# Optimization experiments

Hardware: AMD Instinct MI355X
Metric: run time of the kernel (lower is better)

The kernel has to match this reference:

```python
import jax, jax.numpy as jnp
import numpy as np

B, S, H = 32, 2048, 1024

def setup_inputs() -> dict:
    key = jax.random.key(0)
    k1, k2, k3, k4 = jax.random.split(key, 4)
    scale_w = 1.0 / np.sqrt(3 * H)
    scale_v = 1.0 / np.sqrt(H)
    return {
        "enc_output": jax.random.normal(k1, (B, S, 2 * H), dtype=jnp.float32),
        "enc_mask": jnp.ones((B, S, 1), dtype=jnp.float32),
        "dec_hidden": jax.random.normal(k2, (1, B, H), dtype=jnp.float32),
        "W_w": jax.random.normal(k3, (H, 3 * H), dtype=jnp.float32) * scale_w,
        "W_b": jnp.zeros((H,), dtype=jnp.float32),
        "V_w": jax.random.normal(k4, (1, H), dtype=jnp.float32) * scale_v,
        "V_b": jnp.zeros((1,), dtype=jnp.float32),
    }


def reference(enc_output, enc_mask, dec_hidden, W_w, W_b, V_w, V_b):
    # enc_output: (B, S, 2H); enc_mask: (B, S, 1); dec_hidden: (1, B, H)
    b, s, _ = enc_output.shape
    h = dec_hidden.shape[-1]
    dec = jnp.broadcast_to(jnp.transpose(dec_hidden, (1, 0, 2)), (b, s, h))  # (B,S,H)
    x = jnp.concatenate([enc_output, dec], axis=-1)                          # (B,S,3H)
    energy = jnp.tanh(jnp.einsum('bsk,hk->bsh', x, W_w) + W_b)               # (B,S,H)
    scores = jnp.einsum('bsh,oh->bso', energy, V_w)[..., 0] + V_b[0]         # (B,S)
    keep = enc_mask[..., 0] > 0  # original masks where (1 - mask) is True
    scores = jnp.where(keep, scores, -jnp.inf)
    attn = jax.nn.softmax(scores, axis=-1)                                   # (B,S)
    context = jnp.einsum('bs,bsd->bd', attn, enc_output)                     # (B,2H)
    return context
```

## Files before the change

### kernel.cpp

```cpp
#include <hip/hip_runtime.h>
#include <hip/hip_bf16.h>
#include <math.h>

#define B_   32
#define S_   2048
#define H_   1024
#define K2H  2048
#define M_TOT (B_*S_)

typedef __attribute__((ext_vector_type(8))) short bf16x8;
typedef __attribute__((ext_vector_type(4))) float f32x4;

__device__ __forceinline__ short f2bf(float f) {
    union { float f; unsigned u; } c; c.f = f;
    unsigned u = c.u;
    unsigned r = u + 0x7FFFu + ((u >> 16) & 1u);
    return (short)(r >> 16);
}

__global__ void convert_enc(const float* __restrict__ enc, short* __restrict__ encb) {
    size_t e = ((size_t)blockIdx.x * blockDim.x + threadIdx.x) * 8;
    float4 v0 = *reinterpret_cast<const float4*>(enc + e);
    float4 v1 = *reinterpret_cast<const float4*>(enc + e + 4);
    short s[8];
    s[0]=f2bf(v0.x); s[1]=f2bf(v0.y); s[2]=f2bf(v0.z); s[3]=f2bf(v0.w);
    s[4]=f2bf(v1.x); s[5]=f2bf(v1.y); s[6]=f2bf(v1.z); s[7]=f2bf(v1.w);
    *reinterpret_cast<int4*>(encb + e) = *reinterpret_cast<const int4*>(s);
}

__global__ void convert_w1(const float* __restrict__ W, short* __restrict__ w1) {
    int idx = blockIdx.x * blockDim.x + threadIdx.x;
    int e = idx * 4;
    int h = e >> 11;
    int k = e & 2047;
    float4 v = *reinterpret_cast<const float4*>(W + (size_t)h * 3072 + k);
    short4 o;
    o.x = f2bf(v.x); o.y = f2bf(v.y); o.z = f2bf(v.z); o.w = f2bf(v.w);
    *reinterpret_cast<short4*>(w1 + (size_t)h * 2048 + k) = o;
}

__global__ void dproj_kernel(const float* __restrict__ dec, const float* __restrict__ W,
                             const float* __restrict__ Wb, float* __restrict__ dproj) {
    __shared__ float dl[1024];
    int b = blockIdx.x >> 4;
    int hc = blockIdx.x & 15;
    int t = threadIdx.x;
    for (int i = t; i < 1024; i += 256) dl[i] = dec[b * 1024 + i];
    __syncthreads();
    int wv = t >> 6, lane = t & 63;
    for (int it = 0; it < 16; ++it) {
        int h = hc * 64 + wv * 16 + it;
        const float* wrow = W + (size_t)h * 3072 + 2048;
        float acc = 0.f;
        for (int j = lane; j < 1024; j += 64) acc += dl[j] * wrow[j];
        for (int m = 32; m >= 1; m >>= 1) acc += __shfl_xor(acc, m);
        if (lane == 0) dproj[b * 1024 + h] = acc + Wb[h];
    }
}

#define BM 128
#define BN 128
#define BK 64

__device__ __forceinline__ void gload16(const short* g, short* l) {
    __builtin_amdgcn_global_load_lds(
        (const __attribute__((address_space(1))) void*)g,
        (__attribute__((address_space(3))) void*)l,
        16, 0, 0);
}

__launch_bounds__(256, 4)
__global__ void fused_gemm_lds(const short* __restrict__ encb, const short* __restrict__ w1,
                               const float* __restrict__ dproj, const float* __restrict__ Vw,
                               float* __restrict__ scores_p) {
    __shared__ short As[BM * BK];
    __shared__ short Bs[BN * BK];
    int bid = blockIdx.x;
    int x  = bid & 7;
    int r  = bid >> 3;
    int nt = r & 7;
    int mt = ((r >> 3) << 3) | x;
    int m0 = mt * BM, n0 = nt * BN;
    int t = threadIdx.x, lane = t & 63, wv = t >> 6;
    int wm = wv >> 1, wn = wv & 1;

    int srow = (lane >> 3);
    int scol = (lane & 7) * 8;
    const short* abase = encb + (size_t)m0 * K2H + scol;
    const short* bbase = w1 + (size_t)n0 * K2H + scol;

    f32x4 acc[4][4] = {};

    const int NT = K2H / BK;
    for (int kt = 0; kt < NT; ++kt) {
        __syncthreads();
#pragma unroll
        for (int p = 0; p < 4; ++p) {
            int rr = (p * 4 + wv) * 8 + srow;
            gload16(abase + (size_t)rr * K2H + kt * BK, &As[(p * 4 + wv) * 512]);
            gload16(bbase + (size_t)rr * K2H + kt * BK, &Bs[(p * 4 + wv) * 512]);
        }
        __syncthreads();
#pragma unroll
        for (int ks = 0; ks < 2; ++ks) {
            bf16x8 af[4], bfrag[4];
#pragma unroll
            for (int i = 0; i < 4; ++i)
                af[i] = *reinterpret_cast<const bf16x8*>(
                    &As[(wm * 64 + i * 16 + (lane & 15)) * BK + ks * 32 + (lane >> 4) * 8]);
#pragma unroll
            for (int j = 0; j < 4; ++j)
                bfrag[j] = *reinterpret_cast<const bf16x8*>(
                    &Bs[(wn * 64 + j * 16 + (lane & 15)) * BK + ks * 32 + (lane >> 4) * 8]);
#pragma unroll
            for (int i = 0; i < 4; ++i)
#pragma unroll
                for (int j = 0; j < 4; ++j)
                    acc[i][j] = __builtin_amdgcn_mfma_f32_16x16x32_bf16(af[i], bfrag[j], acc[i][j], 0, 0, 0);
        }
    }

    int b = m0 >> 11;
    float dp[4], vv[4];
#pragma unroll
    for (int j = 0; j < 4; ++j) {
        int hg = n0 + wn * 64 + j * 16 + (lane & 15);
        dp[j] = dproj[b * 1024 + hg];
        vv[j] = Vw[hg];
    }
    float* sp = scores_p + (size_t)(nt * 2 + wn) * M_TOT;
#pragma unroll
    for (int i = 0; i < 4; ++i) {
#pragma unroll
        for (int q = 0; q < 4; ++q) {
            float part = 0.f;
#pragma unroll
            for (int j = 0; j < 4; ++j)
                part += vv[j] * tanhf(acc[i][j][q] + dp[j]);
            part += __shfl_xor(part, 1);
            part += __shfl_xor(part, 2);
            part += __shfl_xor(part, 4);
            part += __shfl_xor(part, 8);
            if ((lane & 15) == 0) {
                int mg = m0 + wm * 64 + i * 16 + ((lane >> 4) << 2) + q;
                sp[mg] = part;
            }
        }
    }
}

#define LDA 72
__launch_bounds__(256, 2)
__global__ void fused_gemm(const float* __restrict__ enc, const short* __restrict__ w1,
                           const float* __restrict__ dproj, const float* __restrict__ Vw,
                           float* __restrict__ scores_p) {
    __shared__ short As[BM * LDA];
    __shared__ short Bs[BN * LDA];
    int bid = blockIdx.x;
    int x  = bid & 7;
    int r  = bid >> 3;
    int nt = r & 7;
    int mt = ((r >> 3) << 3) | x;
    int m0 = mt * BM, n0 = nt * BN;
    int t = threadIdx.x, lane = t & 63, wv = t >> 6;
    int wm = wv >> 1, wn = wv & 1;

    int ar = t >> 4;
    int ac = (t & 15) * 4;
    const float* aptr = enc + (size_t)(m0 + ar) * K2H + ac;
    int br = t >> 3;
    int bc = (t & 7) * 8;
    const short* bptr = w1 + (size_t)(n0 + br) * K2H + bc;

    float4 areg[8];
    int4 breg[4];

    auto loadA = [&](int kt) {
#pragma unroll
        for (int p = 0; p < 8; ++p)
            areg[p] = *reinterpret_cast<const float4*>(aptr + (size_t)(p * 16) * K2H + kt * BK);
    };
    auto loadB = [&](int kt) {
#pragma unroll
        for (int p = 0; p < 4; ++p)
            breg[p] = *reinterpret_cast<const int4*>(bptr + (size_t)(p * 32) * K2H + kt * BK);
    };

    f32x4 acc[4][4] = {};

    loadA(0); loadB(0);
    const int NT = K2H / BK;
    for (int kt = 0; kt < NT; ++kt) {
        __syncthreads();
#pragma unroll
        for (int p = 0; p < 8; ++p) {
            short4 o;
            o.x = f2bf(areg[p].x); o.y = f2bf(areg[p].y);
            o.z = f2bf(areg[p].z); o.w = f2bf(areg[p].w);
            *reinterpret_cast<short4*>(&As[(ar + p * 16) * LDA + ac]) = o;
        }
#pragma unroll
        for (int p = 0; p < 4; ++p)
            *reinterpret_cast<int4*>(&Bs[(br + p * 32) * LDA + bc]) = breg[p];
        __syncthreads();
        if (kt + 1 < NT) { loadA(kt + 1); loadB(kt + 1); }
#pragma unroll
        for (int ks = 0; ks < 2; ++ks) {
            bf16x8 af[4], bfrag[4];
#pragma unroll
            for (int i = 0; i < 4; ++i)
                af[i] = *reinterpret_cast<const bf16x8*>(
                    &As[(wm * 64 + i * 16 + (lane & 15)) * LDA + ks * 32 + (lane >> 4) * 8]);
#pragma unroll
            for (int j = 0; j < 4; ++j)
                bfrag[j] = *reinterpret_cast<const bf16x8*>(
                    &Bs[(wn * 64 + j * 16 + (lane & 15)) * LDA + ks * 32 + (lane >> 4) * 8]);
#pragma unroll
            for (int i = 0; i < 4; ++i)
#pragma unroll
                for (int j = 0; j < 4; ++j)
                    acc[i][j] = __builtin_amdgcn_mfma_f32_16x16x32_bf16(af[i], bfrag[j], acc[i][j], 0, 0, 0);
        }
    }

    int b = m0 >> 11;
    float dp[4], vv[4];
#pragma unroll
    for (int j = 0; j < 4; ++j) {
        int hg = n0 + wn * 64 + j * 16 + (lane & 15);
        dp[j] = dproj[b * 1024 + hg];
        vv[j] = Vw[hg];
    }
    float* sp = scores_p + (size_t)(nt * 2 + wn) * M_TOT;
#pragma unroll
    for (int i = 0; i < 4; ++i) {
#pragma unroll
        for (int q = 0; q < 4; ++q) {
            float part = 0.f;
#pragma unroll
            for (int j = 0; j < 4; ++j)
                part += vv[j] * tanhf(acc[i][j][q] + dp[j]);
            part += __shfl_xor(part, 1);
            part += __shfl_xor(part, 2);
            part += __shfl_xor(part, 4);
            part += __shfl_xor(part, 8);
            if ((lane & 15) == 0) {
                int mg = m0 + wm * 64 + i * 16 + ((lane >> 4) << 2) + q;
                sp[mg] = part;
            }
        }
    }
}

__global__ void softmax_kernel(const float* __restrict__ scores_p, const float* __restrict__ mask,
                               float* __restrict__ attn) {
    int b = blockIdx.x;
    int t = threadIdx.x;
    __shared__ float red[8];
    __shared__ float red2[8];
    float v[8];
    float mx = -INFINITY;
#pragma unroll
    for (int k = 0; k < 8; ++k) {
        int s = t + k * 256;
        float xv = 0.f;
#pragma unroll
        for (int p = 0; p < 16; ++p) xv += scores_p[(size_t)p * M_TOT + b * 2048 + s];
        float mk = mask[b * 2048 + s];
        xv = (mk > 0.f) ? xv : -INFINITY;
        v[k] = xv;
        mx = fmaxf(mx, xv);
    }
    int lane = t & 63, wv = t >> 6;
    for (int m = 32; m >= 1; m >>= 1) mx = fmaxf(mx, __shfl_xor(mx, m));
    if (lane == 0) red[wv] = mx;
    __syncthreads();
    mx = fmaxf(fmaxf(red[0], red[1]), fmaxf(red[2], red[3]));
    float sum = 0.f;
#pragma unroll
    for (int k = 0; k < 8; ++k) { v[k] = __expf(v[k] - mx); sum += v[k]; }
    for (int m = 32; m >= 1; m >>= 1) sum += __shfl_xor(sum, m);
    if (lane == 0) red2[wv] = sum;
    __syncthreads();
    sum = red2[0] + red2[1] + red2[2] + red2[3];
    float inv = 1.f / sum;
#pragma unroll
    for (int k = 0; k < 8; ++k) attn[b * 2048 + t + k * 256] = v[k] * inv;
}

#define SCH 64
__global__ void context_kernel(const float* __restrict__ enc, const float* __restrict__ attn,
                               float* __restrict__ out) {
    int bid = blockIdx.x;
    int b = bid >> 6;
    int dchunk = (bid >> 5) & 1;
    int schunk = bid & 31;
    int t = threadIdx.x;
    __shared__ float aw[SCH];
    if (t < SCH) aw[t] = attn[b * 2048 + schunk * SCH + t];
    __syncthreads();
    int c = dchunk * 1024 + t * 4;
    const float* base = enc + (size_t)b * S_ * K2H + (size_t)(schunk * SCH) * K2H + c;
    float4 acc = {0.f, 0.f, 0.f, 0.f};
    for (int s = 0; s < SCH; ++s) {
        float w = aw[s];
        float4 v = *reinterpret_cast<const float4*>(base + (size_t)s * K2H);
        acc.x += w * v.x; acc.y += w * v.y; acc.z += w * v.z; acc.w += w * v.w;
    }
    float* o = out + b * 2048 + c;
    atomicAdd(o + 0, acc.x);
    atomicAdd(o + 1, acc.y);
    atomicAdd(o + 2, acc.z);
    atomicAdd(o + 3, acc.w);
}

extern "C" void kernel_launch(void* const* d_in, const int* in_sizes, int n_in,
                              void* d_out, int out_size, void* d_ws, size_t ws_size,
                              hipStream_t stream) {
    const float* enc  = (const float*)d_in[0];
    const float* mask = (const float*)d_in[1];
    const float* dec  = (const float*)d_in[2];
    const float* Ww   = (const float*)d_in[3];
    const float* Wb   = (const float*)d_in[4];
    const float* Vw   = (const float*)d_in[5];
    float* out = (float*)d_out;

    char* ws = (char*)d_ws;
    const size_t ENC_B = (size_t)M_TOT * K2H * 2;
    const size_t need  = ENC_B + (4u << 20) + (4u << 20) + (1u << 20);

    hipMemsetAsync(out, 0, (size_t)out_size * sizeof(float), stream);

    if (ws_size >= need) {
        short* encb     = (short*)ws;
        short* w1       = (short*)(ws + ENC_B);
        float* scores_p = (float*)(ws + ENC_B + (4u << 20));
        float* dproj    = (float*)(ws + ENC_B + (8u << 20));
        float* attn     = (float*)(ws + ENC_B + (8u << 20) + (128u << 10));

        convert_enc<<<65536, 256, 0, stream>>>(enc, encb);
        convert_w1<<<2048, 256, 0, stream>>>(Ww, w1);
        dproj_kernel<<<512, 256, 0, stream>>>(dec, Ww, Wb, dproj);
        fused_gemm_lds<<<4096, 256, 0, stream>>>(encb, w1, dproj, Vw, scores_p);
        softmax_kernel<<<32, 256, 0, stream>>>(scores_p, mask, attn);
        context_kernel<<<2048, 256, 0, stream>>>(enc, attn, out);
    } else {
        short* w1       = (short*)ws;
        float* scores_p = (float*)(ws + (4u << 20));
        float* dproj    = (float*)(ws + (8u << 20));
        float* attn     = (float*)(ws + (8u << 20) + (128u << 10));

        convert_w1<<<2048, 256, 0, stream>>>(Ww, w1);
        dproj_kernel<<<512, 256, 0, stream>>>(dec, Ww, Wb, dproj);
        fused_gemm<<<4096, 256, 0, stream>>>(enc, w1, dproj, Vw, scores_p);
        softmax_kernel<<<32, 256, 0, stream>>>(scores_p, mask, attn);
        context_kernel<<<2048, 256, 0, stream>>>(enc, attn, out);
    }
}
```

Measured before the change: 676.3 us.

## Replace GEMM with 256x256 tile, 8-wave, 4-stage pipelined LDS-direct kernel

Replaces the 128x128 single-buffered bf16 MFMA GEMM with a 256x256-tile kernel using 512 threads and a 4-deep ring of LDS buffers. The ring is filled by global_load_lds with explicit vmcnt waits, so global loads overlap compute. An XOR swizzle on LDS columns is meant to avoid bank conflicts, and s_setprio raises priority around the MFMA bursts. The larger tile cuts global and LDS traffic per flop, at the cost of one block per CU and more register pressure from 32 accumulators.

```diff
diff --git a/kernel.cpp b/kernel.cpp
--- a/kernel.cpp
+++ b/kernel.cpp
@@ -16,6 +16,19 @@
     unsigned u = c.u;
     unsigned r = u + 0x7FFFu + ((u >> 16) & 1u);
     return (short)(r >> 16);
+}
+
+__device__ __forceinline__ void bar() {
+    asm volatile("" ::: "memory");
+    __builtin_amdgcn_s_barrier();
+    asm volatile("" ::: "memory");
+}
+
+__device__ __forceinline__ void gload16(const short* g, short* l) {
+    __builtin_amdgcn_global_load_lds(
+        (const __attribute__((address_space(1))) void*)g,
+        (__attribute__((address_space(3))) void*)l,
+        16, 0, 0);
 }
 
 __global__ void convert_enc(const float* __restrict__ enc, short* __restrict__ encb) {
@@ -58,97 +71,131 @@
     }
 }
 
-#define BM 128
-#define BN 128
-#define BK 64
-
-__device__ __forceinline__ void gload16(const short* g, short* l) {
-    __builtin_amdgcn_global_load_lds(
-        (const __attribute__((address_space(1))) void*)g,
-        (__attribute__((address_space(3))) void*)l,
-        16, 0, 0);
-}
-
-__launch_bounds__(256, 4)
-__global__ void fused_gemm_lds(const short* __restrict__ encb, const short* __restrict__ w1,
-                               const float* __restrict__ dproj, const float* __restrict__ Vw,
-                               float* __restrict__ scores_p) {
-    __shared__ short As[BM * BK];
-    __shared__ short Bs[BN * BK];
+__launch_bounds__(512, 1)
+__global__ void fused_gemm8(const short* __restrict__ encb, const short* __restrict__ w1,
+                            const float* __restrict__ dproj, const float* __restrict__ Vw,
+                            float* __restrict__ scores_p) {
+    __shared__ short As[4 * 256 * 32];
+    __shared__ short Bs[4 * 256 * 32];
     int bid = blockIdx.x;
-    int x  = bid & 7;
-    int r  = bid >> 3;
-    int nt = r & 7;
-    int mt = ((r >> 3) << 3) | x;
-    int m0 = mt * BM, n0 = nt * BN;
-    int t = threadIdx.x, lane = t & 63, wv = t >> 6;
-    int wm = wv >> 1, wn = wv & 1;
-
-    int srow = (lane >> 3);
-    int scol = (lane & 7) * 8;
-    const short* abase = encb + (size_t)m0 * K2H + scol;
-    const short* bbase = w1 + (size_t)n0 * K2H + scol;
-
-    f32x4 acc[4][4] = {};
-
-    const int NT = K2H / BK;
-    for (int kt = 0; kt < NT; ++kt) {
-        __syncthreads();
-#pragma unroll
-        for (int p = 0; p < 4; ++p) {
-            int rr = (p * 4 + wv) * 8 + srow;
-            gload16(abase + (size_t)rr * K2H + kt * BK, &As[(p * 4 + wv) * 512]);
-            gload16(bbase + (size_t)rr * K2H + kt * BK, &Bs[(p * 4 + wv) * 512]);
-        }
-        __syncthreads();
-#pragma unroll
-        for (int ks = 0; ks < 2; ++ks) {
-            bf16x8 af[4], bfrag[4];
-#pragma unroll
-            for (int i = 0; i < 4; ++i)
-                af[i] = *reinterpret_cast<const bf16x8*>(
-                    &As[(wm * 64 + i * 16 + (lane & 15)) * BK + ks * 32 + (lane >> 4) * 8]);
-#pragma unroll
-            for (int j = 0; j < 4; ++j)
-                bfrag[j] = *reinterpret_cast<const bf16x8*>(
-                    &Bs[(wn * 64 + j * 16 + (lane & 15)) * BK + ks * 32 + (lane >> 4) * 8]);
-#pragma unroll
-            for (int i = 0; i < 4; ++i)
-#pragma unroll
-                for (int j = 0; j < 4; ++j)
-                    acc[i][j] = __builtin_amdgcn_mfma_f32_16x16x32_bf16(af[i], bfrag[j], acc[i][j], 0, 0, 0);
-        }
+    int x = bid & 7, r = bid >> 3;
+    int nt = r & 3;
+    int mt = ((r >> 2) << 3) | x;
+    int m0 = mt * 256, n0 = nt * 256;
+    int t5 = threadIdx.x, lane = t5 & 63, wv = t5 >> 6;
+    int wm = wv >> 2, wn = wv & 3;
+
+    int sr = t5 >> 2;
+    int sc = t5 & 3;
+
+    auto stA = [&](int kt, int buf) {
+#pragma unroll
+        for (int u = 0; u < 2; ++u) {
+            int lr = u * 128 + sr;
+            int cs = (sc ^ ((lr >> 1) & 3)) * 8;
+            gload16(encb + (size_t)(m0 + lr) * K2H + kt * 32 + cs,
+                    &As[buf * 8192 + lr * 32 + sc * 8]);
+        }
+    };
+    auto stB = [&](int kt, int buf) {
+#pragma unroll
+        for (int u = 0; u < 2; ++u) {
+            int lr = u * 128 + sr;
+            int cs = (sc ^ ((lr >> 1) & 3)) * 8;
+            gload16(w1 + (size_t)(n0 + lr) * K2H + kt * 32 + cs,
+                    &Bs[buf * 8192 + lr * 32 + sc * 8]);
+        }
+    };
+
+    f32x4 acc[8][4] = {};
+    bf16x8 aF[4], aG[4], bF[4];
+
+    stA(0, 0); stB(0, 0);
+    stA(1, 1); stB(1, 1);
+    stA(2, 2); stB(2, 2);
+    asm volatile("s_waitcnt vmcnt(8)" ::: "memory");
+    bar();
+
+    const int NT = 64;
+    for (int t = 0; t < NT; ++t) {
+        int cur = t & 3;
+        const short* Ac = &As[cur * 8192];
+        const short* Bc = &Bs[cur * 8192];
+#pragma unroll
+        for (int ii = 0; ii < 4; ++ii) {
+            int R = wm * 128 + ii * 16 + (lane & 15);
+            aF[ii] = *reinterpret_cast<const bf16x8*>(
+                &Ac[R * 32 + (((lane >> 4) ^ ((R >> 1) & 3)) * 8)]);
+        }
+#pragma unroll
+        for (int jj = 0; jj < 4; ++jj) {
+            int R = wn * 64 + jj * 16 + (lane & 15);
+            bF[jj] = *reinterpret_cast<const bf16x8*>(
+                &Bc[R * 32 + (((lane >> 4) ^ ((R >> 1) & 3)) * 8)]);
+        }
+        if (t <= NT - 4) stA(t + 3, (t + 3) & 3);
+        bar();
+        __builtin_amdgcn_s_setprio(1);
+#pragma unroll
+        for (int ii = 0; ii < 4; ++ii)
+#pragma unroll
+            for (int jj = 0; jj < 4; ++jj)
+                acc[ii][jj] = __builtin_amdgcn_mfma_f32_16x16x32_bf16(aF[ii], bF[jj], acc[ii][jj], 0, 0, 0);
+        __builtin_amdgcn_s_setprio(0);
+        bar();
+#pragma unroll
+        for (int ii = 0; ii < 4; ++ii) {
+            int R = wm * 128 + 64 + ii * 16 + (lane & 15);
+            aG[ii] = *reinterpret_cast<const bf16x8*>(
+                &Ac[R * 32 + (((lane >> 4) ^ ((R >> 1) & 3)) * 8)]);
+        }
+        if (t <= NT - 4) stB(t + 3, (t + 3) & 3);
+        if (t <= NT - 4)      { asm volatile("s_waitcnt vmcnt(8)" ::: "memory"); }
+        else if (t == NT - 3) { asm volatile("s_waitcnt vmcnt(4)" ::: "memory"); }
+        else if (t == NT - 2) { asm volatile("s_waitcnt vmcnt(0)" ::: "memory"); }
+        bar();
+        __builtin_amdgcn_s_setprio(1);
+#pragma unroll
+        for (int ii = 0; ii < 4; ++ii)
+#pragma unroll
+            for (int jj = 0; jj < 4; ++jj)
+                acc[4 + ii][jj] = __builtin_amdgcn_mfma_f32_16x16x32_bf16(aG[ii], bF[jj], acc[4 + ii][jj], 0, 0, 0);
+        __builtin_amdgcn_s_setprio(0);
+        bar();
     }
 
     int b = m0 >> 11;
-    float dp[4], vv[4];
+    float dp[4], vvv[4];
 #pragma unroll
     for (int j = 0; j < 4; ++j) {
         int hg = n0 + wn * 64 + j * 16 + (lane & 15);
         dp[j] = dproj[b * 1024 + hg];
-        vv[j] = Vw[hg];
-    }
-    float* sp = scores_p + (size_t)(nt * 2 + wn) * M_TOT;
-#pragma unroll
-    for (int i = 0; i < 4; ++i) {
+        vvv[j] = Vw[hg];
+    }
+    float* sp = scores_p + (size_t)(nt * 4 + wn) * M_TOT;
+#pragma unroll
+    for (int i = 0; i < 8; ++i) {
 #pragma unroll
         for (int q = 0; q < 4; ++q) {
             float part = 0.f;
 #pragma unroll
             for (int j = 0; j < 4; ++j)
-                part += vv[j] * tanhf(acc[i][j][q] + dp[j]);
+                part += vvv[j] * tanhf(acc[i][j][q] + dp[j]);
             part += __shfl_xor(part, 1);
             part += __shfl_xor(part, 2);
             part += __shfl_xor(part, 4);
             part += __shfl_xor(part, 8);
             if ((lane & 15) == 0) {
-                int mg = m0 + wm * 64 + i * 16 + ((lane >> 4) << 2) + q;
+                int mg = m0 + wm * 128 + i * 16 + ((lane >> 4) << 2) + q;
                 sp[mg] = part;
             }
         }
     }
 }
 
+#define BM 128
+#define BN 128
+#define BK 64
 #define LDA 72
 __launch_bounds__(256, 2)
 __global__ void fused_gemm(const float* __restrict__ enc, const short* __restrict__ w1,
@@ -341,7 +388,7 @@
         convert_enc<<<65536, 256, 0, stream>>>(enc, encb);
         convert_w1<<<2048, 256, 0, stream>>>(Ww, w1);
         dproj_kernel<<<512, 256, 0, stream>>>(dec, Ww, Wb, dproj);
-        fused_gemm_lds<<<4096, 256, 0, stream>>>(encb, w1, dproj, Vw, scores_p);
+        fused_gemm8<<<1024, 512, 0, stream>>>(encb, w1, dproj, Vw, scores_p);
         softmax_kernel<<<32, 256, 0, stream>>>(scores_p, mask, attn);
         context_kernel<<<2048, 256, 0, stream>>>(enc, attn, out);
     } else {
```

Result: no change. 686.3 us (+1.5%).
